# Performance work log

Measured on AMD Instinct MI355X. Metric: run time of the kernel, lower is better.

Reference implementation:

```python
import jax, jax.numpy as jnp
import numpy as np

DECAY = 0.95

def setup_inputs() -> dict:
    key = jax.random.key(0)
    k1, k2, k3, k4 = jax.random.split(key, 4)
    B, S, H, Dk, Dv = 4, 4096, 16, 64, 64
    return {
        "memory": jax.random.normal(k1, (H, Dk, Dv), dtype=jnp.float32),
        "keys": jax.random.normal(k2, (B, S, H, Dk), dtype=jnp.float32),
        "values": jax.random.normal(k3, (B, S, H, Dv), dtype=jnp.float32),
        "write_strengths": jax.random.uniform(k4, (B, S), dtype=jnp.float32),
    }

def reference(memory, keys, values, write_strengths):
    # M_new = decay * M + sum_{b,s} rho[b,s] * k[b,s,h] v[b,s,h]^T
    # Algebraically equivalent to per-head (rho-weighted) K^T V contraction;
    # avoids materializing the (B,S,H,Dk,Dv) outer-product tensor.
    delta = jnp.einsum('bs,bshk,bshv->hkv', write_strengths, keys, values)
    return DECAY * memory + delta
```

## Files before the change

### kernel.cpp

```cpp
#include <hip/hip_runtime.h>
#include <stdint.h>


typedef __bf16  bf16x8  __attribute__((ext_vector_type(8)));
typedef __bf16  bf16x4  __attribute__((ext_vector_type(4)));
typedef short   s16x4   __attribute__((ext_vector_type(4)));
typedef float   floatx4 __attribute__((ext_vector_type(4)));

constexpr int HH   = 16;
constexpr int DK   = 64;
constexpr int DV   = 64;
constexpr int ROWS = 16384;
constexpr int NSLICE = 128;
constexpr int RPB  = ROWS / NSLICE;
constexpr int TR   = 32;
constexpr int NR   = RPB / TR;
constexpr float DECAY = 0.95f;
constexpr size_t WS_NEED = (size_t)NSLICE * HH * DK * DV * sizeof(float);

__global__ __launch_bounds__(256) void init_out(const float* __restrict__ mem,
                                                float* __restrict__ out) {
    int i = blockIdx.x * 256 + threadIdx.x;
    out[i] = DECAY * mem[i];
}

__device__ __forceinline__ unsigned lds_off(const void* p) {
    return (unsigned)(uintptr_t)(__attribute__((address_space(3))) const void*)p;
}

template <bool TWOSTAGE>
__global__ __launch_bounds__(256, 8) void accum(const float* __restrict__ keys,
                                                const float* __restrict__ values,
                                                const float* __restrict__ rho,
                                                float* __restrict__ dst) {
    __shared__ __align__(128) __bf16 kb[2][TR * DK];
    __shared__ __align__(128) __bf16 vb[2][TR * DV];
    __shared__ float rs[RPB];

    const int t    = threadIdx.x;
    const int lane = t & 63;
    const int w    = t >> 6;
    const int wr   = w >> 1;
    const int wc   = w & 1;
    const int m    = lane & 15;
    const int q    = lane >> 4;
    const int h    = blockIdx.y;
    const int row0 = blockIdx.x * RPB;

    if (t < RPB) rs[t] = rho[row0 + t];

    const int sl0 = t >> 4;
    const int c0  = (t & 15) * 4;

    float4 pk[2][2], pv[2][2];

    auto loadr = [&](int r, int set) {
        #pragma unroll
        for (int i = 0; i < 2; ++i) {
            const int sl = sl0 + i * 16;
            const size_t off = ((size_t)(row0 + r * TR + sl) * HH + h) * DK + c0;
            pk[set][i] = *(const float4*)(keys + off);
            pv[set][i] = *(const float4*)(values + off);
        }
    };
    auto writer = [&](int r, int set, int b) {
        #pragma unroll
        for (int i = 0; i < 2; ++i) {
            const int sl = sl0 + i * 16;
            const float rv = rs[r * TR + sl];
            bf16x4 kh = {(__bf16)(pk[set][i].x * rv), (__bf16)(pk[set][i].y * rv),
                         (__bf16)(pk[set][i].z * rv), (__bf16)(pk[set][i].w * rv)};
            bf16x4 vh = {(__bf16)pv[set][i].x, (__bf16)pv[set][i].y,
                         (__bf16)pv[set][i].z, (__bf16)pv[set][i].w};
            const int eo = ((sl >> 2) * 4 + (c0 >> 4)) * 64 + (sl & 3) * 16 + (c0 & 15);
            *(bf16x4*)&kb[b][eo] = kh;
            *(bf16x4*)&vb[b][eo] = vh;
        }
    };

    floatx4 acc[2][2];
    #pragma unroll
    for (int i = 0; i < 2; ++i)
        #pragma unroll
        for (int j = 0; j < 2; ++j)
            acc[i][j] = (floatx4){0.f, 0.f, 0.f, 0.f};

    loadr(0, 0);
    loadr(1, 1);
    __syncthreads();
    writer(0, 0, 0);

    for (int r = 0; r < NR; ++r) {
        const int cur = r & 1;
        __syncthreads();

        const unsigned abase = lds_off(&kb[cur][0]) + q * 1024 + 8 * m;
        const unsigned bbase = lds_off(&vb[cur][0]) + q * 1024 + 8 * m;

        s16x4 alo[2], ahi[2], blo[2], bhi[2];
        #pragma unroll
        for (int mt = 0; mt < 2; ++mt) {
            const unsigned ad = abase + (unsigned)((wr * 2 + mt) * 128);
            asm volatile("ds_read_b64_tr_b16 %0, %1" : "=v"(alo[mt]) : "v"(ad));
            asm volatile("ds_read_b64_tr_b16 %0, %1 offset:512" : "=v"(ahi[mt]) : "v"(ad));
        }
        #pragma unroll
        for (int nt = 0; nt < 2; ++nt) {
            const unsigned bd = bbase + (unsigned)((wc * 2 + nt) * 128);
            asm volatile("ds_read_b64_tr_b16 %0, %1" : "=v"(blo[nt]) : "v"(bd));
            asm volatile("ds_read_b64_tr_b16 %0, %1 offset:512" : "=v"(bhi[nt]) : "v"(bd));
        }

        if (r + 2 < NR) loadr(r + 2, cur);

        asm volatile("s_waitcnt lgkmcnt(0)" ::: "memory");
        __builtin_amdgcn_sched_barrier(0);

        bf16x8 af[2], bfv[2];
        #pragma unroll
        for (int mt = 0; mt < 2; ++mt) {
            union { s16x4 hh[2]; bf16x8 v; } u;
            u.hh[0] = alo[mt]; u.hh[1] = ahi[mt];
            af[mt] = u.v;
        }
        #pragma unroll
        for (int nt = 0; nt < 2; ++nt) {
            union { s16x4 hh[2]; bf16x8 v; } u;
            u.hh[0] = blo[nt]; u.hh[1] = bhi[nt];
            bfv[nt] = u.v;
        }

        #pragma unroll
        for (int mt = 0; mt < 2; ++mt)
            #pragma unroll
            for (int nt = 0; nt < 2; ++nt)
                acc[mt][nt] = __builtin_amdgcn_mfma_f32_16x16x32_bf16(
                    af[mt], bfv[nt], acc[mt][nt], 0, 0, 0);

        if (r + 1 < NR) writer(r + 1, (r + 1) & 1, (r + 1) & 1);
    }

    if (TWOSTAGE) {
        float* o = dst + ((size_t)(blockIdx.x * HH + h)) * (DK * DV)
                       + (wr * 32) * DV + wc * 32;
        #pragma unroll
        for (int mt = 0; mt < 2; ++mt)
            #pragma unroll
            for (int nt = 0; nt < 2; ++nt)
                #pragma unroll
                for (int g = 0; g < 4; ++g)
                    o[(mt * 16 + q * 4 + g) * DV + nt * 16 + m] = acc[mt][nt][g];
    } else {
        float* o = dst + h * (DK * DV) + (wr * 32) * DV + wc * 32;
        #pragma unroll
        for (int mt = 0; mt < 2; ++mt)
            #pragma unroll
            for (int nt = 0; nt < 2; ++nt)
                #pragma unroll
                for (int g = 0; g < 4; ++g)
                    atomicAdd(o + (mt * 16 + q * 4 + g) * DV + nt * 16 + m,
                              acc[mt][nt][g]);
    }
}

__global__ __launch_bounds__(256) void reduce_ws(const float* __restrict__ ws,
                                                 float* __restrict__ out) {
    constexpr int SLAB = HH * DK * DV / 4;
    constexpr int QS   = NSLICE / 4;
    const int tid = blockIdx.x * 256 + threadIdx.x;
    const int i4  = tid & (SLAB - 1);
    const int qu  = tid >> 14;
    const floatx4* wv = (const floatx4*)ws;
    floatx4 s0 = {0.f, 0.f, 0.f, 0.f}, s1 = {0.f, 0.f, 0.f, 0.f};
    #pragma unroll 8
    for (int sl = 0; sl < QS; sl += 2) {
        s0 += wv[(size_t)(qu * QS + sl) * SLAB + i4];
        s1 += wv[(size_t)(qu * QS + sl + 1) * SLAB + i4];
    }
    s0 += s1;
    float* o = out + i4 * 4;
    atomicAdd(o + 0, s0.x);
    atomicAdd(o + 1, s0.y);
    atomicAdd(o + 2, s0.z);
    atomicAdd(o + 3, s0.w);
}

extern "C" void kernel_launch(void* const* d_in, const int* in_sizes, int n_in,
                              void* d_out, int out_size, void* d_ws, size_t ws_size,
                              hipStream_t stream) {
    const float* mem    = (const float*)d_in[0];
    const float* keys   = (const float*)d_in[1];
    const float* values = (const float*)d_in[2];
    const float* rho    = (const float*)d_in[3];
    float* out = (float*)d_out;

    dim3 grid(NSLICE, HH);
    init_out<<<dim3((HH * DK * DV) / 256), dim3(256), 0, stream>>>(mem, out);
    if (ws_size >= WS_NEED) {
        accum<true><<<grid, dim3(256), 0, stream>>>(keys, values, rho, (float*)d_ws);
        reduce_ws<<<dim3(256), dim3(256), 0, stream>>>((const float*)d_ws, out);
    } else {
        accum<false><<<grid, dim3(256), 0, stream>>>(keys, values, rho, out);
    }
}
```

Before: 191.3 us.

## Process eight heads per block with one wave per head for contiguous loads

Each 512-thread block now covers 8 heads of one row slice, and each wave computes a full 64x64 head tile. Previously each block handled one head with four waves splitting the tile. Per-row loads become 2KB contiguous spans across the heads instead of 256B strided fragments, which improves global coalescing. The block count drops from 2048 to 256, register pressure rises with 16 accumulators and 8 prefetched float4 pairs per thread, and prefetch depth drops from two stages to one.

```diff
diff --git a/kernel.cpp b/kernel.cpp
--- a/kernel.cpp
+++ b/kernel.cpp
@@ -15,6 +15,7 @@
 constexpr int RPB  = ROWS / NSLICE;
 constexpr int TR   = 32;
 constexpr int NR   = RPB / TR;
+constexpr int HPB  = 8;
 constexpr float DECAY = 0.95f;
 constexpr size_t WS_NEED = (size_t)NSLICE * HH * DK * DV * sizeof(float);
 
@@ -29,133 +30,130 @@
 }
 
 template <bool TWOSTAGE>
-__global__ __launch_bounds__(256, 8) void accum(const float* __restrict__ keys,
+__global__ __launch_bounds__(512, 2) void accum(const float* __restrict__ keys,
                                                 const float* __restrict__ values,
                                                 const float* __restrict__ rho,
                                                 float* __restrict__ dst) {
-    __shared__ __align__(128) __bf16 kb[2][TR * DK];
-    __shared__ __align__(128) __bf16 vb[2][TR * DV];
+    __shared__ __align__(128) __bf16 kb[2][HPB][TR * DK];
+    __shared__ __align__(128) __bf16 vb[2][HPB][TR * DV];
     __shared__ float rs[RPB];
 
     const int t    = threadIdx.x;
     const int lane = t & 63;
     const int w    = t >> 6;
-    const int wr   = w >> 1;
-    const int wc   = w & 1;
     const int m    = lane & 15;
     const int q    = lane >> 4;
-    const int h    = blockIdx.y;
-    const int row0 = blockIdx.x * RPB;
+    const int h0   = blockIdx.x * HPB;
+    const int slice = blockIdx.y;
+    const int row0 = slice * RPB;
 
     if (t < RPB) rs[t] = rho[row0 + t];
 
-    const int sl0 = t >> 4;
-    const int c0  = (t & 15) * 4;
-
-    float4 pk[2][2], pv[2][2];
-
-    auto loadr = [&](int r, int set) {
-        #pragma unroll
-        for (int i = 0; i < 2; ++i) {
-            const int sl = sl0 + i * 16;
-            const size_t off = ((size_t)(row0 + r * TR + sl) * HH + h) * DK + c0;
-            pk[set][i] = *(const float4*)(keys + off);
-            pv[set][i] = *(const float4*)(values + off);
+    const int fc  = t & 127;
+    const int rg  = t >> 7;
+    const int hh  = fc >> 4;
+    const int cl4 = fc & 15;
+
+    float4 pk[8], pv[8];
+
+    auto loadr = [&](int r) {
+        const float* kp = keys   + (size_t)(row0 + r * TR + rg) * (HH * DK) + h0 * DK + fc * 4;
+        const float* vp = values + (size_t)(row0 + r * TR + rg) * (HH * DV) + h0 * DV + fc * 4;
+        #pragma unroll
+        for (int i = 0; i < 8; ++i) {
+            pk[i] = *(const float4*)(kp + (size_t)i * 4 * (HH * DK));
+            pv[i] = *(const float4*)(vp + (size_t)i * 4 * (HH * DV));
         }
     };
-    auto writer = [&](int r, int set, int b) {
-        #pragma unroll
-        for (int i = 0; i < 2; ++i) {
-            const int sl = sl0 + i * 16;
+    auto writer = [&](int r, int b) {
+        #pragma unroll
+        for (int i = 0; i < 8; ++i) {
+            const int sl = rg + i * 4;
             const float rv = rs[r * TR + sl];
-            bf16x4 kh = {(__bf16)(pk[set][i].x * rv), (__bf16)(pk[set][i].y * rv),
-                         (__bf16)(pk[set][i].z * rv), (__bf16)(pk[set][i].w * rv)};
-            bf16x4 vh = {(__bf16)pv[set][i].x, (__bf16)pv[set][i].y,
-                         (__bf16)pv[set][i].z, (__bf16)pv[set][i].w};
-            const int eo = ((sl >> 2) * 4 + (c0 >> 4)) * 64 + (sl & 3) * 16 + (c0 & 15);
-            *(bf16x4*)&kb[b][eo] = kh;
-            *(bf16x4*)&vb[b][eo] = vh;
+            bf16x4 kh = {(__bf16)(pk[i].x * rv), (__bf16)(pk[i].y * rv),
+                         (__bf16)(pk[i].z * rv), (__bf16)(pk[i].w * rv)};
+            bf16x4 vh = {(__bf16)pv[i].x, (__bf16)pv[i].y,
+                         (__bf16)pv[i].z, (__bf16)pv[i].w};
+            const int eo = ((sl >> 2) * 4 + (cl4 >> 2)) * 64 + (sl & 3) * 16 + (cl4 & 3) * 4;
+            *(bf16x4*)&kb[b][hh][eo] = kh;
+            *(bf16x4*)&vb[b][hh][eo] = vh;
         }
     };
 
-    floatx4 acc[2][2];
+    floatx4 acc[4][4];
     #pragma unroll
-    for (int i = 0; i < 2; ++i)
-        #pragma unroll
-        for (int j = 0; j < 2; ++j)
+    for (int i = 0; i < 4; ++i)
+        #pragma unroll
+        for (int j = 0; j < 4; ++j)
             acc[i][j] = (floatx4){0.f, 0.f, 0.f, 0.f};
 
-    loadr(0, 0);
-    loadr(1, 1);
+    loadr(0);
     __syncthreads();
-    writer(0, 0, 0);
+    writer(0, 0);
 
     for (int r = 0; r < NR; ++r) {
         const int cur = r & 1;
+        if (r + 1 < NR) loadr(r + 1);
         __syncthreads();
 
-        const unsigned abase = lds_off(&kb[cur][0]) + q * 1024 + 8 * m;
-        const unsigned bbase = lds_off(&vb[cur][0]) + q * 1024 + 8 * m;
-
-        s16x4 alo[2], ahi[2], blo[2], bhi[2];
-        #pragma unroll
-        for (int mt = 0; mt < 2; ++mt) {
-            const unsigned ad = abase + (unsigned)((wr * 2 + mt) * 128);
+        const unsigned abase = lds_off(&kb[cur][w][0]) + q * 1024 + 8 * m;
+        const unsigned bbase = lds_off(&vb[cur][w][0]) + q * 1024 + 8 * m;
+
+        s16x4 alo[4], ahi[4], blo[4], bhi[4];
+        #pragma unroll
+        for (int mt = 0; mt < 4; ++mt) {
+            const unsigned ad = abase + (unsigned)(mt * 128);
             asm volatile("ds_read_b64_tr_b16 %0, %1" : "=v"(alo[mt]) : "v"(ad));
             asm volatile("ds_read_b64_tr_b16 %0, %1 offset:512" : "=v"(ahi[mt]) : "v"(ad));
         }
         #pragma unroll
-        for (int nt = 0; nt < 2; ++nt) {
-            const unsigned bd = bbase + (unsigned)((wc * 2 + nt) * 128);
+        for (int nt = 0; nt < 4; ++nt) {
+            const unsigned bd = bbase + (unsigned)(nt * 128);
             asm volatile("ds_read_b64_tr_b16 %0, %1" : "=v"(blo[nt]) : "v"(bd));
             asm volatile("ds_read_b64_tr_b16 %0, %1 offset:512" : "=v"(bhi[nt]) : "v"(bd));
         }
-
-        if (r + 2 < NR) loadr(r + 2, cur);
-
         asm volatile("s_waitcnt lgkmcnt(0)" ::: "memory");
         __builtin_amdgcn_sched_barrier(0);
 
-        bf16x8 af[2], bfv[2];
-        #pragma unroll
-        for (int mt = 0; mt < 2; ++mt) {
-            union { s16x4 hh[2]; bf16x8 v; } u;
-            u.hh[0] = alo[mt]; u.hh[1] = ahi[mt];
+        bf16x8 af[4], bfv[4];
+        #pragma unroll
+        for (int mt = 0; mt < 4; ++mt) {
+            union { s16x4 hh2[2]; bf16x8 v; } u;
+            u.hh2[0] = alo[mt]; u.hh2[1] = ahi[mt];
             af[mt] = u.v;
         }
         #pragma unroll
-        for (int nt = 0; nt < 2; ++nt) {
-            union { s16x4 hh[2]; bf16x8 v; } u;
-            u.hh[0] = blo[nt]; u.hh[1] = bhi[nt];
+        for (int nt = 0; nt < 4; ++nt) {
+            union { s16x4 hh2[2]; bf16x8 v; } u;
+            u.hh2[0] = blo[nt]; u.hh2[1] = bhi[nt];
             bfv[nt] = u.v;
         }
 
         #pragma unroll
-        for (int mt = 0; mt < 2; ++mt)
+        for (int mt = 0; mt < 4; ++mt)
             #pragma unroll
-            for (int nt = 0; nt < 2; ++nt)
+            for (int nt = 0; nt < 4; ++nt)
                 acc[mt][nt] = __builtin_amdgcn_mfma_f32_16x16x32_bf16(
                     af[mt], bfv[nt], acc[mt][nt], 0, 0, 0);
 
-        if (r + 1 < NR) writer(r + 1, (r + 1) & 1, (r + 1) & 1);
+        if (r + 1 < NR) writer(r + 1, cur ^ 1);
     }
 
     if (TWOSTAGE) {
-        float* o = dst + ((size_t)(blockIdx.x * HH + h)) * (DK * DV)
-                       + (wr * 32) * DV + wc * 32;
-        #pragma unroll
-        for (int mt = 0; mt < 2; ++mt)
+        float* o = dst + ((size_t)slice * HH + (h0 + w)) * (DK * DV);
+        #pragma unroll
+        for (int mt = 0; mt < 4; ++mt)
             #pragma unroll
-            for (int nt = 0; nt < 2; ++nt)
+            for (int nt = 0; nt < 4; ++nt)
                 #pragma unroll
                 for (int g = 0; g < 4; ++g)
                     o[(mt * 16 + q * 4 + g) * DV + nt * 16 + m] = acc[mt][nt][g];
     } else {
-        float* o = dst + h * (DK * DV) + (wr * 32) * DV + wc * 32;
-        #pragma unroll
-        for (int mt = 0; mt < 2; ++mt)
+        float* o = dst + (size_t)(h0 + w) * (DK * DV);
+        #pragma unroll
+        for (int mt = 0; mt < 4; ++mt)
             #pragma unroll
-            for (int nt = 0; nt < 2; ++nt)
+            for (int nt = 0; nt < 4; ++nt)
                 #pragma unroll
                 for (int g = 0; g < 4; ++g)
                     atomicAdd(o + (mt * 16 + q * 4 + g) * DV + nt * 16 + m,
@@ -194,12 +192,12 @@
     const float* rho    = (const float*)d_in[3];
     float* out = (float*)d_out;
 
-    dim3 grid(NSLICE, HH);
+    dim3 grid(2, NSLICE);
     init_out<<<dim3((HH * DK * DV) / 256), dim3(256), 0, stream>>>(mem, out);
     if (ws_size >= WS_NEED) {
-        accum<true><<<grid, dim3(256), 0, stream>>>(keys, values, rho, (float*)d_ws);
+        accum<true><<<grid, dim3(512), 0, stream>>>(keys, values, rho, (float*)d_ws);
         reduce_ws<<<dim3(256), dim3(256), 0, stream>>>((const float*)d_ws, out);
     } else {
-        accum<false><<<grid, dim3(256), 0, stream>>>(keys, values, rho, out);
-    }
-}
+        accum<false><<<grid, dim3(512), 0, stream>>>(keys, values, rho, out);
+    }
+}
```

New measurement: 168.0 us. 1.14x faster.
